# Performance work log

Hardware: AMD Instinct MI355X
Metric: run time of the kernel (lower is better)

The kernel has to match this reference:

```python
import jax, jax.numpy as jnp
import numpy as np

N, T, FS, FD, GH, RH, E = 100000, 24, 32, 8, 32, 64, 3200000


def spmm(edge_row, edge_col, edge_val, X):
    # out[i] = sum_e val[e] * X[col[e]]  for edges with row[e]==i
    return jax.ops.segment_sum(edge_val[:, None] * X[edge_col], edge_row, num_segments=N)


def setup_inputs() -> dict:
    key = jax.random.key(0)
    ks = jax.random.split(key, 20)
    s = 0.05
    return {
        "X_static": jax.random.normal(ks[0], (N, FS), jnp.float32),
        "X_dyn_mean": jax.random.normal(ks[1], (T, N, FD), jnp.float32),
        "edge_row": jax.random.randint(ks[2], (E,), 0, N, jnp.int32),
        "edge_col": jax.random.randint(ks[3], (E,), 0, N, jnp.int32),
        "edge_val": jax.random.uniform(ks[4], (E,), jnp.float32),
        # GraphConv layers
        "g1_W": jax.random.normal(ks[5], (GH, FS), jnp.float32) * s,
        "g1_b": jnp.zeros((GH,), jnp.float32),
        "g2_W": jax.random.normal(ks[6], (GH, GH), jnp.float32) * s,
        "g2_b": jnp.zeros((GH,), jnp.float32),
        # GRU (PyTorch layout: 3H rows = [r, z, n])
        "W_ih": jax.random.normal(ks[7], (3 * RH, GH + FD), jnp.float32) * s,
        "W_hh": jax.random.normal(ks[8], (3 * RH, RH), jnp.float32) * s,
        "b_ih": jnp.zeros((3 * RH,), jnp.float32),
        "b_hh": jnp.zeros((3 * RH,), jnp.float32),
        # MLP head
        "h1_W": jax.random.normal(ks[9], (64, RH), jnp.float32) * s,
        "h1_b": jnp.zeros((64,), jnp.float32),
        "h2_W": jax.random.normal(ks[10], (1, 64), jnp.float32) * s,
        "h2_b": jnp.zeros((1,), jnp.float32),
    }


def reference(X_static, X_dyn_mean, edge_row, edge_col, edge_val,
              g1_W, g1_b, g2_W, g2_b, W_ih, W_hh, b_ih, b_hh,
              h1_W, h1_b, h2_W, h2_b):
    # GraphConv x2: linear then sparse A_hat @ Xw, ReLU
    h = jax.nn.relu(spmm(edge_row, edge_col, edge_val, X_static @ g1_W.T + g1_b))
    h = jax.nn.relu(spmm(edge_row, edge_col, edge_val, h @ g2_W.T + g2_b))  # (N, GH)

    # z_t = concat([h, X_dyn_mean[t]], -1); precompute input-gate projections
    z_seq = jnp.concatenate([jnp.broadcast_to(h[None], (T, N, GH)), X_dyn_mean], axis=-1)  # (T,N,GH+FD)
    gi_all = jnp.einsum('tnd,hd->tnh', z_seq, W_ih) + b_ih  # (T,N,3H)

    def step(hs, gi):
        gh = hs @ W_hh.T + b_hh
        i_r, i_z, i_n = jnp.split(gi, 3, axis=-1)
        h_r, h_z, h_n = jnp.split(gh, 3, axis=-1)
        r = jax.nn.sigmoid(i_r + h_r)
        zg = jax.nn.sigmoid(i_z + h_z)
        n = jnp.tanh(i_n + r * h_n)
        h_new = (1.0 - zg) * n + zg * hs
        return h_new, h_new

    h0 = jnp.zeros((N, RH), jnp.float32)
    _, out = jax.lax.scan(step, h0, gi_all)  # (T,N,RH)

    y = jax.nn.relu(out @ h1_W.T + h1_b)
    y = jax.nn.sigmoid(y @ h2_W.T + h2_b)[..., 0]  # (T,N)
    return y
```

## Files before the change

kernel.cpp:

```cpp
#include <hip/hip_runtime.h>
#include <math.h>

typedef short bf16x8_t __attribute__((ext_vector_type(8)));
typedef float f32x4_t  __attribute__((ext_vector_type(4)));

__device__ __forceinline__ float fast_rcp(float x) { return __builtin_amdgcn_rcpf(x); }
__device__ __forceinline__ float sigmoidf_(float x) {
  return fast_rcp(1.0f + __expf(-x));
}
__device__ __forceinline__ float tanhf_(float x) {
  return fmaf(-2.0f, fast_rcp(__expf(2.0f * x) + 1.0f), 1.0f);
}
__device__ __forceinline__ unsigned short f2bf(float f) {
  unsigned int u = __float_as_uint(f);
  unsigned int r = (u + 0x7fffu + ((u >> 16) & 1u)) >> 16;
  return (unsigned short)r;
}
__device__ __forceinline__ float bf2f(unsigned short u) {
  return __uint_as_float(((unsigned int)u) << 16);
}
__device__ __forceinline__ unsigned int cvt_pk_bf16(float a, float b) {
  unsigned int d;
  asm("v_cvt_pk_bf16_f32 %0, %1, %2" : "=v"(d) : "v"(a), "v"(b));
  return d;
}

template<bool RELU_IN, bool OUT_BF16>
__global__ __launch_bounds__(256) void lin32_kernel(
    const float* __restrict__ X, const float* __restrict__ W,
    const float* __restrict__ b, void* __restrict__ outp, int N)
{
  __shared__ float sW[32][33];
  __shared__ float sb[32];
  __shared__ float sX[8][33];
  const int tid = threadIdx.x;
  for (int i = tid; i < 1024; i += 256) sW[i >> 5][i & 31] = W[i];
  if (tid < 32) sb[tid] = b[tid];
  const int n0 = blockIdx.x * 8;
  {
    float v = X[(size_t)n0 * 32 + tid];
    if (RELU_IN) v = fmaxf(v, 0.0f);
    sX[tid >> 5][tid & 31] = v;
  }
  __syncthreads();
  const int ln = tid >> 5, f = tid & 31;
  float acc = sb[f];
  #pragma unroll
  for (int j = 0; j < 32; j++) acc += sX[ln][j] * sW[f][j];
  if (OUT_BF16) ((unsigned short*)outp)[(size_t)n0 * 32 + tid] = f2bf(acc);
  else          ((float*)outp)[(size_t)n0 * 32 + tid] = acc;
}

__global__ __launch_bounds__(256) void spmm_kernel(
    const int* __restrict__ erow, const int* __restrict__ ecol,
    const float* __restrict__ eval, const float* __restrict__ X,
    float* __restrict__ out, int E)
{
  const long gid = (long)blockIdx.x * 256 + threadIdx.x;
  const int e = (int)(gid >> 3);
  const int q = (int)(gid & 7);
  if (e >= E) return;
  const int r = erow[e], c = ecol[e];
  const float v = eval[e];
  const float4 x = *(const float4*)(X + (size_t)c * 32 + q * 4);
  float* o = out + (size_t)r * 32 + q * 4;
  atomicAdd(o + 0, v * x.x);
  atomicAdd(o + 1, v * x.y);
  atomicAdd(o + 2, v * x.z);
  atomicAdd(o + 3, v * x.w);
}

#define BROWS 128
#define BSHIFT 7
#define EPB 8192
#define MAXBUCKETS 1024

__global__ __launch_bounds__(256) void hist_bin_k(
    const int* __restrict__ erow, int* __restrict__ blockHist,
    int E, int nBuckets)
{
  __shared__ int h[MAXBUCKETS];
  for (int i = threadIdx.x; i < nBuckets; i += 256) h[i] = 0;
  __syncthreads();
  const int e0 = blockIdx.x * EPB;
  const int cnt = min(E - e0, EPB);
  for (int i = threadIdx.x; i < cnt; i += 256)
    atomicAdd(&h[erow[e0 + i] >> BSHIFT], 1);
  __syncthreads();
  int* o = blockHist + (size_t)blockIdx.x * nBuckets;
  for (int i = threadIdx.x; i < nBuckets; i += 256) o[i] = h[i];
}

__global__ __launch_bounds__(1024) void scan_bin_k(
    int* __restrict__ blockHist, int* __restrict__ bucketStart,
    int nb, int nBuckets)
{
  __shared__ int s[1024];
  const int b = threadIdx.x;
  int run = 0;
  if (b < nBuckets) {
    for (int blk = 0; blk < nb; blk++) {
      int* p = blockHist + (size_t)blk * nBuckets + b;
      int t = *p;
      *p = run;
      run += t;
    }
  }
  s[b] = run;
  __syncthreads();
  for (int off = 1; off < 1024; off <<= 1) {
    int u = (b >= off) ? s[b - off] : 0;
    __syncthreads(); s[b] += u; __syncthreads();
  }
  if (b < nBuckets) bucketStart[b] = s[b] - run;
  if (b == nBuckets - 1) bucketStart[nBuckets] = s[b];
}

__global__ __launch_bounds__(256) void scatter_bin_k(
    const int* __restrict__ erow, const int* __restrict__ ecol,
    const float* __restrict__ evl, const int* __restrict__ blockOfs,
    const int* __restrict__ bucketStart, int2* __restrict__ binned,
    int E, int nBuckets)
{
  __shared__ int cur[MAXBUCKETS];
  const int* ofs = blockOfs + (size_t)blockIdx.x * nBuckets;
  for (int i = threadIdx.x; i < nBuckets; i += 256)
    cur[i] = bucketStart[i] + ofs[i];
  __syncthreads();
  const int e0 = blockIdx.x * EPB;
  const int cnt = min(E - e0, EPB);
  for (int i = threadIdx.x; i < cnt; i += 256) {
    int r = erow[e0 + i];
    int c = ecol[e0 + i];
    float v = evl[e0 + i];
    int p = atomicAdd(&cur[r >> BSHIFT], 1);
    binned[p] = make_int2(((r & (BROWS - 1)) << 17) | c, __float_as_int(v));
  }
}

__global__ __launch_bounds__(512) void bucket_sort_k(
    const int* __restrict__ bucketStart, const int2* __restrict__ binned,
    int2* __restrict__ pairs, int* __restrict__ startv, int* __restrict__ cnt,
    int N)
{
  __shared__ int h[BROWS], sc[BROWS], cur[BROWS];
  const int tid = threadIdx.x;
  const int bkt = blockIdx.x;
  const int s = bucketStart[bkt], e = bucketStart[bkt + 1];
  if (tid < BROWS) h[tid] = 0;
  __syncthreads();
  for (int i = s + tid; i < e; i += 512)
    atomicAdd(&h[((unsigned)binned[i].x) >> 17], 1);
  __syncthreads();
  if (tid < BROWS) sc[tid] = h[tid];
  __syncthreads();
  #pragma unroll
  for (int off = 1; off < BROWS; off <<= 1) {
    int u = (tid < BROWS && tid >= off) ? sc[tid - off] : 0;
    __syncthreads();
    if (tid < BROWS) sc[tid] += u;
    __syncthreads();
  }
  if (tid < BROWS) {
    int start = s + sc[tid] - h[tid];
    cur[tid] = start;
    int row = (bkt << BSHIFT) + tid;
    if (row < N) { startv[row] = start; cnt[row] = h[tid]; }
  }
  __syncthreads();
  for (int i = s + tid; i < e; i += 512) {
    int2 r = binned[i];
    int p = atomicAdd(&cur[((unsigned)r.x) >> 17], 1);
    pairs[p] = make_int2(r.x & 0x1ffff, r.y);
  }
}

__global__ __launch_bounds__(256) void hist_k(const int* __restrict__ erow, int* cnt, int E) {
  int e = blockIdx.x * 256 + threadIdx.x;
  if (e < E) atomicAdd(&cnt[erow[e]], 1);
}

__global__ __launch_bounds__(256) void scan1_k(const int* __restrict__ cnt, int* startv, int* bsum, int N) {
  __shared__ int s[256];
  int t = threadIdx.x, i = blockIdx.x * 256 + t;
  int v = (i < N) ? cnt[i] : 0;
  s[t] = v; __syncthreads();
  for (int off = 1; off < 256; off <<= 1) {
    int u = (t >= off) ? s[t - off] : 0;
    __syncthreads(); s[t] += u; __syncthreads();
  }
  if (i < N) startv[i] = s[t] - v;
  if (t == 255) bsum[blockIdx.x] = s[255];
}

__global__ __launch_bounds__(512) void scan2_k(const int* __restrict__ bsum, int* bsumx, int nb) {
  __shared__ int s[512];
  int t = threadIdx.x;
  int v = (t < nb) ? bsum[t] : 0;
  s[t] = v; __syncthreads();
  for (int off = 1; off < 512; off <<= 1) {
    int u = (t >= off) ? s[t - off] : 0;
    __syncthreads(); s[t] += u; __syncthreads();
  }
  if (t < nb) bsumx[t] = s[t] - v;
}

__global__ __launch_bounds__(256) void scan3_k(int* startv, const int* __restrict__ bsumx, int* cursor, int N) {
  int i = blockIdx.x * 256 + threadIdx.x;
  if (i < N) {
    int v = startv[i] + bsumx[i >> 8];
    startv[i] = v;
    cursor[i] = v;
  }
}

__global__ __launch_bounds__(256) void scatter_k(
    const int* __restrict__ erow, const int* __restrict__ ecol,
    const float* __restrict__ evl, int* cursor, int2* __restrict__ pairs, int E)
{
  int e = blockIdx.x * 256 + threadIdx.x;
  if (e < E) {
    int r = erow[e];
    int p = atomicAdd(&cursor[r], 1);
    pairs[p] = make_int2(ecol[e], __float_as_int(evl[e]));
  }
}

__global__ __launch_bounds__(256) void spmm_csr_bf16_k(
    const int* __restrict__ startv, const int* __restrict__ cnt,
    const int2* __restrict__ pairs, const unsigned short* __restrict__ X,
    float* __restrict__ out, int N)
{
  int row = blockIdx.x * 4 + (threadIdx.x >> 6);
  if (row >= N) return;
  int lane = threadIdx.x & 63;
  int f = lane & 31, hh = lane >> 5;
  int start = startv[row];
  int len = cnt[row];
  int half = len >> 1;
  int base = start + (hh ? half : 0);
  int n = hh ? (len - half) : half;
  float acc = 0.0f;
  int i = 0;
  for (; i + 7 < n; i += 8) {
    int2 p0 = pairs[base + i + 0];
    int2 p1 = pairs[base + i + 1];
    int2 p2 = pairs[base + i + 2];
    int2 p3 = pairs[base + i + 3];
    int2 p4 = pairs[base + i + 4];
    int2 p5 = pairs[base + i + 5];
    int2 p6 = pairs[base + i + 6];
    int2 p7 = pairs[base + i + 7];
    float x0 = bf2f(X[(size_t)p0.x * 32 + f]);
    float x1 = bf2f(X[(size_t)p1.x * 32 + f]);
    float x2 = bf2f(X[(size_t)p2.x * 32 + f]);
    float x3 = bf2f(X[(size_t)p3.x * 32 + f]);
    float x4 = bf2f(X[(size_t)p4.x * 32 + f]);
    float x5 = bf2f(X[(size_t)p5.x * 32 + f]);
    float x6 = bf2f(X[(size_t)p6.x * 32 + f]);
    float x7 = bf2f(X[(size_t)p7.x * 32 + f]);
    acc = fmaf(__int_as_float(p0.y), x0, acc);
    acc = fmaf(__int_as_float(p1.y), x1, acc);
    acc = fmaf(__int_as_float(p2.y), x2, acc);
    acc = fmaf(__int_as_float(p3.y), x3, acc);
    acc = fmaf(__int_as_float(p4.y), x4, acc);
    acc = fmaf(__int_as_float(p5.y), x5, acc);
    acc = fmaf(__int_as_float(p6.y), x6, acc);
    acc = fmaf(__int_as_float(p7.y), x7, acc);
  }
  for (; i + 3 < n; i += 4) {
    int2 p0 = pairs[base + i + 0];
    int2 p1 = pairs[base + i + 1];
    int2 p2 = pairs[base + i + 2];
    int2 p3 = pairs[base + i + 3];
    float x0 = bf2f(X[(size_t)p0.x * 32 + f]);
    float x1 = bf2f(X[(size_t)p1.x * 32 + f]);
    float x2 = bf2f(X[(size_t)p2.x * 32 + f]);
    float x3 = bf2f(X[(size_t)p3.x * 32 + f]);
    acc = fmaf(__int_as_float(p0.y), x0, acc);
    acc = fmaf(__int_as_float(p1.y), x1, acc);
    acc = fmaf(__int_as_float(p2.y), x2, acc);
    acc = fmaf(__int_as_float(p3.y), x3, acc);
  }
  for (; i < n; i++) {
    int2 p = pairs[base + i];
    acc = fmaf(__int_as_float(p.y), bf2f(X[(size_t)p.x * 32 + f]), acc);
  }
  acc += __shfl_down(acc, 32);
  if (hh == 0) out[(size_t)row * 32 + f] = acc;
}

#define NB 32

__global__ __launch_bounds__(256, 2) void gru_head_mfma(
    const float* __restrict__ acc2,
    const float* __restrict__ xdyn,
    const float* __restrict__ Wih,
    const float* __restrict__ Whh,
    const float* __restrict__ bih, const float* __restrict__ bhh,
    const float* __restrict__ h1W,
    const float* __restrict__ h1b, const float* __restrict__ h2W,
    const float* __restrict__ h2b,
    float* __restrict__ out, int N, int T)
{
  __shared__ __align__(16) unsigned short z[2][NB][104];
  __shared__ float s_red[2][NB][5];

  const int tid  = threadIdx.x;
  const int w    = tid >> 6;
  const int lane = tid & 63;
  const int ml   = lane & 15;
  const int q    = lane >> 4;
  const int n0   = blockIdx.x * NB;

  bf16x8_t A_r[3], A_z[3], A_in, A_hn[2];
  {
    const int j = 16 * w + ml;
    #pragma unroll
    for (int s = 0; s < 3; s++) {
      union { bf16x8_t v; unsigned short u[8]; } tr, tz;
      #pragma unroll
      for (int jj = 0; jj < 8; jj++) {
        int k = s * 32 + q * 8 + jj;
        float vr = (k < 64) ? Whh[j * 64 + k]        : (k < 72 ? Wih[j * 40 + 32 + (k - 64)] : 0.0f);
        float vz = (k < 64) ? Whh[(64 + j) * 64 + k] : (k < 72 ? Wih[(64 + j) * 40 + 32 + (k - 64)] : 0.0f);
        tr.u[jj] = f2bf(vr);
        tz.u[jj] = f2bf(vz);
      }
      A_r[s] = tr.v; A_z[s] = tz.v;
    }
    union { bf16x8_t v; unsigned short u[8]; } ti;
    #pragma unroll
    for (int jj = 0; jj < 8; jj++) {
      int kk = q * 8 + jj;
      ti.u[jj] = f2bf((kk < 8) ? Wih[(128 + j) * 40 + 32 + kk] : 0.0f);
    }
    A_in = ti.v;
    #pragma unroll
    for (int s = 0; s < 2; s++) {
      union { bf16x8_t v; unsigned short u[8]; } th;
      #pragma unroll
      for (int jj = 0; jj < 8; jj++)
        th.u[jj] = f2bf(Whh[(128 + j) * 64 + s * 32 + q * 8 + jj]);
      A_hn[s] = th.v;
    }
  }
  bf16x8_t Ah[2];
  #pragma unroll
  for (int s = 0; s < 2; s++) {
    union { bf16x8_t v; unsigned short u[8]; } tmp;
    #pragma unroll
    for (int jj = 0; jj < 8; jj++)
      tmp.u[jj] = f2bf(h1W[(16 * w + ml) * 64 + s * 32 + q * 8 + jj]);
    Ah[s] = tmp.v;
  }

  f32x4_t bhhn4, h1b4;
  float h2w_r[4];
  #pragma unroll
  for (int reg = 0; reg < 4; reg++) {
    int j = 16 * w + 4 * q + reg;
    bhhn4[reg] = bhh[128 + j];
    h1b4[reg]  = h1b[j];
    h2w_r[reg] = h2W[j];
  }
  const float h2b0 = h2b[0];

  {
    int nd = tid >> 3, f0 = (tid & 7) * 4;
    float4 v = *(const float4*)(acc2 + (size_t)(n0 + nd) * 32 + f0);
    uint2 pk;
    pk.x = cvt_pk_bf16(fmaxf(v.x, 0.0f), fmaxf(v.y, 0.0f));
    pk.y = cvt_pk_bf16(fmaxf(v.z, 0.0f), fmaxf(v.w, 0.0f));
    *(uint2*)&z[0][nd][f0] = pk;
  }
  __syncthreads();

  f32x4_t gis[3][2];
  {
    bf16x8_t Ag[3];
    #pragma unroll
    for (int g = 0; g < 3; g++) {
      union { bf16x8_t v; unsigned short u[8]; } tmp;
      #pragma unroll
      for (int jj = 0; jj < 8; jj++)
        tmp.u[jj] = f2bf(Wih[(g * 64 + 16 * w + ml) * 40 + q * 8 + jj]);
      Ag[g] = tmp.v;
    }
    bf16x8_t Bg[2];
    #pragma unroll
    for (int nt = 0; nt < 2; nt++)
      Bg[nt] = *(const bf16x8_t*)&z[0][nt * 16 + ml][q * 8];
    f32x4_t zero = {0.0f, 0.0f, 0.0f, 0.0f};
    #pragma unroll
    for (int g = 0; g < 3; g++)
      #pragma unroll
      for (int nt = 0; nt < 2; nt++)
        gis[g][nt] = __builtin_amdgcn_mfma_f32_16x16x32_bf16(Ag[g], Bg[nt], zero, 0, 0, 0);
  }
  __syncthreads();

  for (int i = tid; i < 2 * NB * 104 / 2; i += 256) ((unsigned int*)z)[i] = 0;
  #pragma unroll
  for (int reg = 0; reg < 4; reg++) {
    int j = 16 * w + 4 * q + reg;
    float br = bih[j] + bhh[j];
    float bz = bih[64 + j] + bhh[64 + j];
    float bn = bih[128 + j];
    #pragma unroll
    for (int nt = 0; nt < 2; nt++) {
      gis[0][nt][reg] += br;
      gis[1][nt][reg] += bz;
      gis[2][nt][reg] += bn;
    }
  }
  __syncthreads();

  float hreg[2][4] = {{0, 0, 0, 0}, {0, 0, 0, 0}};

  float4 xv = make_float4(0.f, 0.f, 0.f, 0.f);
  if (tid < 64) xv = *(const float4*)(xdyn + (size_t)n0 * 8 + tid * 4);

  for (int t = 0; t < T; t++) {
    const int b = t & 1;
    if (tid < 64) {
      uint2 pk;
      pk.x = cvt_pk_bf16(xv.x, xv.y);
      pk.y = cvt_pk_bf16(xv.z, xv.w);
      *(uint2*)&z[b][tid >> 1][64 + (tid & 1) * 4] = pk;
      if (t + 1 < T)
        xv = *(const float4*)(xdyn + ((size_t)(t + 1) * N + n0) * 8 + tid * 4);
    }
    __syncthreads();

    if (t >= 2 && tid < 32) {
      float s = s_red[1 - b][tid][0] + s_red[1 - b][tid][1] +
                s_red[1 - b][tid][2] + s_red[1 - b][tid][3];
      out[(size_t)(t - 2) * N + n0 + tid] = sigmoidf_(s + h2b0);
    }

    #pragma unroll
    for (int nt = 0; nt < 2; nt++) {
      bf16x8_t B0 = *(const bf16x8_t*)&z[b][nt * 16 + ml][q * 8];
      bf16x8_t B1 = *(const bf16x8_t*)&z[b][nt * 16 + ml][32 + q * 8];
      bf16x8_t B2 = *(const bf16x8_t*)&z[b][nt * 16 + ml][64 + q * 8];

      f32x4_t ar  = gis[0][nt];
      f32x4_t az  = gis[1][nt];
      f32x4_t ain = gis[2][nt];
      f32x4_t ahn = bhhn4;
      ar  = __builtin_amdgcn_mfma_f32_16x16x32_bf16(A_r[0], B0, ar, 0, 0, 0);
      az  = __builtin_amdgcn_mfma_f32_16x16x32_bf16(A_z[0], B0, az, 0, 0, 0);
      ahn = __builtin_amdgcn_mfma_f32_16x16x32_bf16(A_hn[0], B0, ahn, 0, 0, 0);
      ar  = __builtin_amdgcn_mfma_f32_16x16x32_bf16(A_r[1], B1, ar, 0, 0, 0);
      az  = __builtin_amdgcn_mfma_f32_16x16x32_bf16(A_z[1], B1, az, 0, 0, 0);
      ahn = __builtin_amdgcn_mfma_f32_16x16x32_bf16(A_hn[1], B1, ahn, 0, 0, 0);
      ar  = __builtin_amdgcn_mfma_f32_16x16x32_bf16(A_r[2], B2, ar, 0, 0, 0);
      az  = __builtin_amdgcn_mfma_f32_16x16x32_bf16(A_z[2], B2, az, 0, 0, 0);
      ain = __builtin_amdgcn_mfma_f32_16x16x32_bf16(A_in,  B2, ain, 0, 0, 0);

      if (t >= 1) {
        f32x4_t ha = h1b4;
        ha = __builtin_amdgcn_mfma_f32_16x16x32_bf16(Ah[0], B0, ha, 0, 0, 0);
        ha = __builtin_amdgcn_mfma_f32_16x16x32_bf16(Ah[1], B1, ha, 0, 0, 0);
        float p = 0.0f;
        #pragma unroll
        for (int reg = 0; reg < 4; reg++)
          p += h2w_r[reg] * fmaxf(ha[reg], 0.0f);
        p += __shfl_xor(p, 16, 64);
        p += __shfl_xor(p, 32, 64);
        if (q == 0) s_red[b][nt * 16 + ml][w] = p;
      }

      float hv[4];
      #pragma unroll
      for (int reg = 0; reg < 4; reg++) {
        float r  = sigmoidf_(ar[reg]);
        float zg = sigmoidf_(az[reg]);
        float nn = tanhf_(fmaf(r, ahn[reg], ain[reg]));
        float h  = fmaf(zg, hreg[nt][reg] - nn, nn);
        hreg[nt][reg] = h;
        hv[reg] = h;
      }
      uint2 pk;
      pk.x = cvt_pk_bf16(hv[0], hv[1]);
      pk.y = cvt_pk_bf16(hv[2], hv[3]);
      *(uint2*)&z[1 - b][nt * 16 + ml][16 * w + 4 * q] = pk;
    }
  }

  const int bl = (T - 1) & 1;
  __syncthreads();

  if (tid < 32) {
    float s = s_red[bl][tid][0] + s_red[bl][tid][1] +
              s_red[bl][tid][2] + s_red[bl][tid][3];
    out[(size_t)(T - 2) * N + n0 + tid] = sigmoidf_(s + h2b0);
  }
  #pragma unroll
  for (int nt = 0; nt < 2; nt++) {
    bf16x8_t B0 = *(const bf16x8_t*)&z[1 - bl][nt * 16 + ml][q * 8];
    bf16x8_t B1 = *(const bf16x8_t*)&z[1 - bl][nt * 16 + ml][32 + q * 8];
    f32x4_t ha = h1b4;
    ha = __builtin_amdgcn_mfma_f32_16x16x32_bf16(Ah[0], B0, ha, 0, 0, 0);
    ha = __builtin_amdgcn_mfma_f32_16x16x32_bf16(Ah[1], B1, ha, 0, 0, 0);
    float p = 0.0f;
    #pragma unroll
    for (int reg = 0; reg < 4; reg++)
      p += h2w_r[reg] * fmaxf(ha[reg], 0.0f);
    p += __shfl_xor(p, 16, 64);
    p += __shfl_xor(p, 32, 64);
    if (q == 0) s_red[1 - bl][nt * 16 + ml][w] = p;
  }
  __syncthreads();
  if (tid < 32) {
    float s = s_red[1 - bl][tid][0] + s_red[1 - bl][tid][1] +
              s_red[1 - bl][tid][2] + s_red[1 - bl][tid][3];
    out[(size_t)(T - 1) * N + n0 + tid] = sigmoidf_(s + h2b0);
  }
}

extern "C" void kernel_launch(void* const* d_in, const int* in_sizes, int n_in,
                              void* d_out, int out_size, void* d_ws, size_t ws_size,
                              hipStream_t stream) {
  const float* Xs   = (const float*)d_in[0];
  const float* Xd   = (const float*)d_in[1];
  const int*   erow = (const int*)d_in[2];
  const int*   ecol = (const int*)d_in[3];
  const float* evl  = (const float*)d_in[4];
  const float* g1W  = (const float*)d_in[5];
  const float* g1b  = (const float*)d_in[6];
  const float* g2W  = (const float*)d_in[7];
  const float* g2b  = (const float*)d_in[8];
  const float* Wih  = (const float*)d_in[9];
  const float* Whh  = (const float*)d_in[10];
  const float* bih  = (const float*)d_in[11];
  const float* bhh  = (const float*)d_in[12];
  const float* h1W  = (const float*)d_in[13];
  const float* h1b  = (const float*)d_in[14];
  const float* h2W  = (const float*)d_in[15];
  const float* h2b  = (const float*)d_in[16];

  const int N = in_sizes[0] / 32;
  const int E = in_sizes[2];
  const int T = in_sizes[1] / (N * 8);

  float* out  = (float*)d_out;
  char*  base = (char*)d_ws;
  float* buf0 = (float*)base;
  float* buf1 = buf0 + (size_t)N * 32;
  int*   cnt    = (int*)(buf1 + (size_t)N * 32);
  int*   startv = cnt + N;
  int*   cursor = startv + N;
  int*   bsum   = cursor + N;
  int*   bsumx  = bsum + 512;
  unsigned short* buf0h = (unsigned short*)buf0;

  const int nBuckets = (N + BROWS - 1) >> BSHIFT;
  const int nbBin    = (E + EPB - 1) / EPB;

  int* bucketStart = bsumx + 512;
  int* blockHist   = bucketStart + nBuckets + 1;
  char* pp = (char*)(blockHist + (size_t)nbBin * nBuckets);
  pp = (char*)(((uintptr_t)pp + 15) & ~(uintptr_t)15);
  int2* pairs  = (int2*)pp;
  int2* binned = pairs + E;

  const size_t neededA = (size_t)((char*)(binned + E) - base);
  const size_t neededB = (size_t)((char*)(pairs + E) - base);

  const int linBlocks = (N + 7) / 8;
  const int eBlocks   = (E + 255) / 256;
  const int nb1       = (N + 255) / 256;

  const bool tierA = (ws_size >= neededA) && (nBuckets <= MAXBUCKETS) &&
                     (N <= (1 << 17));
  const bool tierB = !tierA && (ws_size >= neededB);

  if (tierA) {
    lin32_kernel<false, true><<<linBlocks, 256, 0, stream>>>(Xs, g1W, g1b, buf0h, N);

    hist_bin_k<<<nbBin, 256, 0, stream>>>(erow, blockHist, E, nBuckets);
    scan_bin_k<<<1, 1024, 0, stream>>>(blockHist, bucketStart, nbBin, nBuckets);
    scatter_bin_k<<<nbBin, 256, 0, stream>>>(erow, ecol, evl, blockHist,
                                             bucketStart, binned, E, nBuckets);
    bucket_sort_k<<<nBuckets, 512, 0, stream>>>(bucketStart, binned, pairs,
                                                startv, cnt, N);

    spmm_csr_bf16_k<<<(N + 3) / 4, 256, 0, stream>>>(startv, cnt, pairs, buf0h, buf1, N);
    lin32_kernel<true, true><<<linBlocks, 256, 0, stream>>>(buf1, g2W, g2b, buf0h, N);
    spmm_csr_bf16_k<<<(N + 3) / 4, 256, 0, stream>>>(startv, cnt, pairs, buf0h, buf1, N);
  } else if (tierB) {
    lin32_kernel<false, true><<<linBlocks, 256, 0, stream>>>(Xs, g1W, g1b, buf0h, N);

    hipMemsetAsync(cnt, 0, (size_t)N * sizeof(int), stream);
    hist_k<<<eBlocks, 256, 0, stream>>>(erow, cnt, E);
    scan1_k<<<nb1, 256, 0, stream>>>(cnt, startv, bsum, N);
    scan2_k<<<1, 512, 0, stream>>>(bsum, bsumx, nb1);
    scan3_k<<<nb1, 256, 0, stream>>>(startv, bsumx, cursor, N);
    scatter_k<<<eBlocks, 256, 0, stream>>>(erow, ecol, evl, cursor, pairs, E);

    spmm_csr_bf16_k<<<(N + 3) / 4, 256, 0, stream>>>(startv, cnt, pairs, buf0h, buf1, N);
    lin32_kernel<true, true><<<linBlocks, 256, 0, stream>>>(buf1, g2W, g2b, buf0h, N);
    spmm_csr_bf16_k<<<(N + 3) / 4, 256, 0, stream>>>(startv, cnt, pairs, buf0h, buf1, N);
  } else {
    lin32_kernel<false, false><<<linBlocks, 256, 0, stream>>>(Xs, g1W, g1b, buf0, N);
    const int spmmBlocks = (int)(((long)E * 8 + 255) / 256);
    hipMemsetAsync(buf1, 0, (size_t)N * 32 * sizeof(float), stream);
    spmm_kernel<<<spmmBlocks, 256, 0, stream>>>(erow, ecol, evl, buf0, buf1, E);
    lin32_kernel<true, false><<<linBlocks, 256, 0, stream>>>(buf1, g2W, g2b, buf0, N);
    hipMemsetAsync(buf1, 0, (size_t)N * 32 * sizeof(float), stream);
    spmm_kernel<<<spmmBlocks, 256, 0, stream>>>(erow, ecol, evl, buf0, buf1, E);
  }

  gru_head_mfma<<<N / NB, 256, 0, stream>>>(buf1, Xd, Wih, Whh, bih, bhh,
                                            h1W, h1b, h2W, h2b, out, N, T);
}
```

Measured before the change: 695.5 us.

## Parallelize per-bucket block-histogram scan across many blocks

Replaces the single-block column scan, where each thread serially walked all block histograms for one bucket, with a kernel that runs one block per bucket. Inside each block, 128 threads split the column into chunks, take local sums and do a shared-memory scan. A second small kernel then computes bucket start offsets from the per-bucket totals. This targets a latency-bound serial loop on one CU, at the cost of one extra launch and a strided memory access pattern.

New measurement: 606.7 us. 12.8% less time.

```diff
diff --git a/kernel.cpp b/kernel.cpp
--- a/kernel.cpp
+++ b/kernel.cpp
@@ -91,28 +91,48 @@
   for (int i = threadIdx.x; i < nBuckets; i += 256) o[i] = h[i];
 }
 
-__global__ __launch_bounds__(1024) void scan_bin_k(
-    int* __restrict__ blockHist, int* __restrict__ bucketStart,
+__global__ __launch_bounds__(128) void colscan_k(
+    int* __restrict__ blockHist, int* __restrict__ bucketTotal,
     int nb, int nBuckets)
+{
+  __shared__ int s[128];
+  const int b = blockIdx.x;
+  const int t = threadIdx.x;
+  const int k = (nb + 127) >> 7;
+  const int i0 = t * k, i1 = min(nb, i0 + k);
+  int p = 0;
+  for (int i = i0; i < i1; i++) p += blockHist[(size_t)i * nBuckets + b];
+  s[t] = p;
+  __syncthreads();
+  #pragma unroll
+  for (int off = 1; off < 128; off <<= 1) {
+    int u = (t >= off) ? s[t - off] : 0;
+    __syncthreads(); s[t] += u; __syncthreads();
+  }
+  int run = s[t] - p;
+  if (t == 127) bucketTotal[b] = s[127];
+  for (int i = i0; i < i1; i++) {
+    int* q = &blockHist[(size_t)i * nBuckets + b];
+    int v = *q;
+    *q = run;
+    run += v;
+  }
+}
+
+__global__ __launch_bounds__(1024) void bucketstart_k(
+    const int* __restrict__ bucketTotal, int* __restrict__ bucketStart,
+    int nBuckets)
 {
   __shared__ int s[1024];
   const int b = threadIdx.x;
-  int run = 0;
-  if (b < nBuckets) {
-    for (int blk = 0; blk < nb; blk++) {
-      int* p = blockHist + (size_t)blk * nBuckets + b;
-      int t = *p;
-      *p = run;
-      run += t;
-    }
-  }
-  s[b] = run;
+  int v = (b < nBuckets) ? bucketTotal[b] : 0;
+  s[b] = v;
   __syncthreads();
   for (int off = 1; off < 1024; off <<= 1) {
     int u = (b >= off) ? s[b - off] : 0;
     __syncthreads(); s[b] += u; __syncthreads();
   }
-  if (b < nBuckets) bucketStart[b] = s[b] - run;
+  if (b < nBuckets) bucketStart[b] = s[b] - v;
   if (b == nBuckets - 1) bucketStart[nBuckets] = s[b];
 }
 
@@ -560,7 +580,8 @@
   const int nbBin    = (E + EPB - 1) / EPB;
 
   int* bucketStart = bsumx + 512;
-  int* blockHist   = bucketStart + nBuckets + 1;
+  int* bucketTotal = bucketStart + nBuckets + 1;
+  int* blockHist   = bucketTotal + nBuckets;
   char* pp = (char*)(blockHist + (size_t)nbBin * nBuckets);
   pp = (char*)(((uintptr_t)pp + 15) & ~(uintptr_t)15);
   int2* pairs  = (int2*)pp;
@@ -581,7 +602,8 @@
     lin32_kernel<false, true><<<linBlocks, 256, 0, stream>>>(Xs, g1W, g1b, buf0h, N);
 
     hist_bin_k<<<nbBin, 256, 0, stream>>>(erow, blockHist, E, nBuckets);
-    scan_bin_k<<<1, 1024, 0, stream>>>(blockHist, bucketStart, nbBin, nBuckets);
+    colscan_k<<<nBuckets, 128, 0, stream>>>(blockHist, bucketTotal, nbBin, nBuckets);
+    bucketstart_k<<<1, 1024, 0, stream>>>(bucketTotal, bucketStart, nBuckets);
     scatter_bin_k<<<nbBin, 256, 0, stream>>>(erow, ecol, evl, blockHist,
                                              bucketStart, binned, E, nBuckets);
     bucket_sort_k<<<nBuckets, 512, 0, stream>>>(bucketStart, binned, pairs,
```
